# Kernel tuning notes

Hardware: AMD Instinct MI355X
Metric: run time of the kernel (lower is better)

## Reference

```python
import jax, jax.numpy as jnp
import numpy as np


def setup_inputs() -> dict:
    key = jax.random.key(0)
    ks = jax.random.split(key, 4)
    B, C, H, W = 4, 512, 64, 64
    A = 512  # attention_dim
    x = jax.random.normal(ks[0], (B, C, H, W), dtype=jnp.float32)
    # 1x1 conv weights as [out_ch, in_ch] matrices (kaiming-like scale)
    scale = np.sqrt(2.0 / C).astype(np.float32)
    Wq = jax.random.normal(ks[1], (A, C), dtype=jnp.float32) * scale
    Wk = jax.random.normal(ks[2], (A, C), dtype=jnp.float32) * scale
    Wv = jax.random.normal(ks[3], (C, C), dtype=jnp.float32) * scale
    bq = jnp.zeros((A,), dtype=jnp.float32)
    bk = jnp.zeros((A,), dtype=jnp.float32)
    bv = jnp.zeros((C,), dtype=jnp.float32)
    return {"x": x, "Wq": Wq, "bq": bq, "Wk": Wk, "bk": bk, "Wv": Wv, "bv": bv}


def reference(x, Wq, bq, Wk, bk, Wv, bv):
    B, C, H, W = x.shape
    N = H * W
    xf = x.reshape(B, C, N)  # [B, C, N]
    # 1x1 convs == per-pixel channel matmuls
    q = jnp.einsum('ac,bcn->bna', Wq, xf) + bq[None, None, :]   # [B, N, A] (query, permuted)
    k = jnp.einsum('ac,bcn->ban', Wk, xf) + bk[None, :, None]   # [B, A, N] (key)
    v = jnp.einsum('oc,bcn->bno', Wv, xf) + bv[None, None, :]   # [B, N, C] (value, permuted)
    attn = jnp.einsum('bna,bam->bnm', q, k)                     # [B, N, N]
    attn = jax.nn.softmax(attn, axis=-2)                        # softmax over dim=-2 (queries)
    out = jnp.einsum('bnm,bmc->bnc', attn, v)                   # [B, N, C]
    # Faithful to torch: .view(B, C, H, W) reinterprets the [B, N, C] buffer
    out = out.reshape(B, C, H, W)
    return x + 0.1 * out
```

## Files before the change

kernel.cpp:

```cpp
#include <hip/hip_runtime.h>
#include <stdint.h>


#define LDT 40
#define SUB 5120

typedef _Float16 f16x8 __attribute__((ext_vector_type(8)));
typedef float f32x4 __attribute__((ext_vector_type(4)));

template <int ASRC, int EPI, int NSUB>
__global__ void __launch_bounds__(256, 2) gemm_f16(
    const _Float16* __restrict__ Ap, long lda, long zsa,
    const _Float16* __restrict__ Bp, long ldb, long zsb,
    int kslice,
    const _Float16* __restrict__ fs16, long zsl,
    float* __restrict__ outF, _Float16* __restrict__ outH, long ldc, long zso,
    const float* __restrict__ bias0, const float* __restrict__ bias1,
    const float* __restrict__ xadd,
    float* __restrict__ pmax, float* __restrict__ psum, long zsp,
    float alpha)
{
  __shared__ _Float16 smem[2 * NSUB * SUB];

  const int z = blockIdx.z;
  const long i0 = (long)blockIdx.x * 128;
  const long j0 = (long)blockIdx.y * 128;
  const int t = (int)threadIdx.x;
  const int lane = t & 63;
  const int wv = t >> 6;
  const int quad = lane >> 4;
  const int lrow = lane & 15;
  const int wm = (wv & 1) << 6;
  const int wn = (wv >> 1) << 6;

  const int r0 = t >> 2;
  const int s0 = (t & 3) << 3;

  const _Float16* gA0 = Ap + z * zsa + (i0 + r0) * lda + s0;
  const _Float16* gA1 = gA0 + 64 * lda;
  const _Float16* gB0 = Bp + z * zsb + (j0 + r0) * ldb + s0;
  const _Float16* gB1 = gB0 + 64 * ldb;
  const int la0 = r0 * LDT + s0;
  const int la1 = (r0 + 64) * LDT + s0;

  const _Float16* fsZ = nullptr;
  if constexpr (ASRC == 1)
    fsZ = fs16 + z * zsl + (long)blockIdx.x * 4096 + s0;

  f32x4 acc[4][4];
  const f32x4 fz = {0.f, 0.f, 0.f, 0.f};
#pragma unroll
  for (int a = 0; a < 4; a++)
#pragma unroll
    for (int b = 0; b < 4; b++) acc[a][b] = fz;

  for (int kk = 0; kk < kslice; kk += 32 * NSUB) {
    f16x8 va[NSUB][2], vb[NSUB][2];
#pragma unroll
    for (int s = 0; s < NSUB; s++) {
      va[s][0] = *(const f16x8*)(gA0 + kk + 32 * s);
      va[s][1] = *(const f16x8*)(gA1 + kk + 32 * s);
      vb[s][0] = *(const f16x8*)(gB0 + kk + 32 * s);
      vb[s][1] = *(const f16x8*)(gB1 + kk + 32 * s);
    }
    if constexpr (ASRC == 1) {
#pragma unroll
      for (int s = 0; s < NSUB; s++) {
        const f16x8 fsv = *(const f16x8*)(fsZ + kk + 32 * s);
        va[s][0] = va[s][0] * fsv;
        va[s][1] = va[s][1] * fsv;
      }
    }
    __syncthreads();
#pragma unroll
    for (int s = 0; s < NSUB; s++) {
      *(f16x8*)&smem[s * SUB + la0] = va[s][0];
      *(f16x8*)&smem[s * SUB + la1] = va[s][1];
      *(f16x8*)&smem[(NSUB + s) * SUB + la0] = vb[s][0];
      *(f16x8*)&smem[(NSUB + s) * SUB + la1] = vb[s][1];
    }
    __syncthreads();

#pragma unroll
    for (int h = 0; h < NSUB; h++) {
      const _Float16* pA = smem + h * SUB;
      const _Float16* pB = smem + (NSUB + h) * SUB;
      f16x8 fa[4], fb[4];
#pragma unroll
      for (int f = 0; f < 4; f++) {
        fa[f] = *(const f16x8*)&pA[(wm + f * 16 + lrow) * LDT + quad * 8];
        fb[f] = *(const f16x8*)&pB[(wn + f * 16 + lrow) * LDT + quad * 8];
      }
#pragma unroll
      for (int fm = 0; fm < 4; fm++)
#pragma unroll
        for (int fn = 0; fn < 4; fn++)
          acc[fm][fn] = __builtin_amdgcn_mfma_f32_16x16x32_f16(fa[fm], fb[fn], acc[fm][fn], 0, 0, 0);
    }
  }

  const long obase = (long)z * zso;

  if constexpr (EPI == 1 || EPI == 2) {
#pragma unroll
    for (int fm = 0; fm < 4; fm++) {
      const long gi0 = i0 + wm + fm * 16 + quad * 4;
#pragma unroll
      for (int fn = 0; fn < 4; fn++) {
        const long gj = j0 + wn + fn * 16 + lrow;
        float badd = 0.f;
        if constexpr (EPI == 1) badd = (gj < 512) ? bias0[gj] : bias1[gj - 512];
#pragma unroll
        for (int r = 0; r < 4; r++) {
          float v = acc[fm][fn][r];
          if constexpr (EPI == 1) v += badd;
          else v += bias0[gi0 + r];
          outH[obase + (gi0 + r) * ldc + gj] = (_Float16)v;
        }
      }
    }
  } else if constexpr (EPI == 3) {
#pragma unroll
    for (int fm = 0; fm < 4; fm++) {
      const long gi0 = i0 + wm + fm * 16 + quad * 4;
#pragma unroll
      for (int fn = 0; fn < 4; fn++) {
        const long gj = j0 + wn + fn * 16 + lrow;
#pragma unroll
        for (int r = 0; r < 4; r++) {
          const long o = obase + (gi0 + r) * ldc + gj;
          outF[o] = fmaf(alpha, acc[fm][fn][r], xadd[o]);
        }
      }
    }
  } else {
    __syncthreads();
    float* Ls = (float*)smem;
#pragma unroll
    for (int fn = 0; fn < 4; fn++) {
      float mx = -3.4e38f;
#pragma unroll
      for (int fm = 0; fm < 4; fm++)
#pragma unroll
        for (int r = 0; r < 4; r++) mx = fmaxf(mx, acc[fm][fn][r]);
      Ls[(wv * 4 + quad) * 64 + fn * 16 + lrow] = mx;
    }
    __syncthreads();
    {
      const int c = t & 127;
      const int h = t >> 7;
      const int wvv = ((c >> 6) << 1) + h;
      const int wc = c & 63;
      float M = -3.4e38f;
#pragma unroll
      for (int q = 0; q < 4; q++) M = fmaxf(M, Ls[(wvv * 4 + q) * 64 + wc]);
      Ls[1024 + h * 128 + c] = M;
    }
    __syncthreads();
    if (t < 128) {
      float Mcol = fmaxf(Ls[1024 + t], Ls[1152 + t]);
      pmax[z * zsp + (long)blockIdx.x * 4096 + j0 + t] = Mcol;
      Ls[1280 + t] = Mcol;
    }
    __syncthreads();
#pragma unroll
    for (int fn = 0; fn < 4; fn++) {
      const int colc = wn + fn * 16 + lrow;
      const float Mcol = Ls[1280 + colc];
      const long gj = j0 + colc;
      float sm = 0.f;
#pragma unroll
      for (int fm = 0; fm < 4; fm++) {
        const long gi0 = i0 + wm + fm * 16 + quad * 4;
#pragma unroll
        for (int r = 0; r < 4; r++) {
          float e = __expf(acc[fm][fn][r] - Mcol);
          sm += e;
          outH[obase + (gi0 + r) * ldc + gj] = (_Float16)e;
        }
      }
      Ls[(wv * 4 + quad) * 64 + fn * 16 + lrow] = sm;
    }
    __syncthreads();
    if (t < 128) {
      const int wc = t & 63;
      const int ch = t >> 6;
      float s = 0.f;
#pragma unroll
      for (int h = 0; h < 2; h++) {
        const int wvv = (ch << 1) + h;
#pragma unroll
        for (int q = 0; q < 4; q++) s += Ls[(wvv * 4 + q) * 64 + wc];
      }
      psum[z * zsp + (long)blockIdx.x * 4096 + j0 + t] = s;
    }
  }
}

__global__ void convert_weights(const float* __restrict__ Wq, const float* __restrict__ Wk,
                                const float* __restrict__ Wv,
                                _Float16* __restrict__ WQK, _Float16* __restrict__ Wv16)
{
  int idx = blockIdx.x * 256 + threadIdx.x;
  if (idx < 524288)
    WQK[idx] = (_Float16)((idx < 262144) ? Wq[idx] : Wk[idx - 262144]);
  else
    Wv16[idx - 524288] = (_Float16)Wv[idx - 524288];
}

__global__ void transpose_x(const float* __restrict__ x, _Float16* __restrict__ xT)
{
  __shared__ float tile[32][33];
  const int b = blockIdx.z;
  const int n0 = blockIdx.x * 32;
  const int c0 = blockIdx.y * 32;
  const int tx = threadIdx.x;
  const int ty = threadIdx.y;
  const float* xb = x + (long)b * 2097152;
#pragma unroll
  for (int k = 0; k < 4; k++)
    tile[ty + k * 8][tx] = xb[(long)(c0 + ty + k * 8) * 4096 + n0 + tx];
  __syncthreads();
  _Float16* xTb = xT + (long)b * 2097152;
#pragma unroll
  for (int k = 0; k < 4; k++)
    xTb[(long)(n0 + ty + k * 8) * 512 + c0 + tx] = (_Float16)tile[tx][ty + k * 8];
}

__global__ void stats_scale(const float* __restrict__ pmax, const float* __restrict__ psum,
                            _Float16* __restrict__ fs16)
{
  const int idx = blockIdx.x * 256 + threadIdx.x;
  const int z = idx >> 12;
  const int m = idx & 4095;
  const float* pm = pmax + (long)z * 131072 + m;
  const float* ps = psum + (long)z * 131072 + m;
  float M = -3.4e38f, S = 0.f;
  for (int i = 0; i < 32; i++) {
    float m2 = pm[(long)i * 4096], s2 = ps[(long)i * 4096];
    float nm = fmaxf(M, m2);
    S = S * __expf(M - nm) + s2 * __expf(m2 - nm);
    M = nm;
  }
  const float lse = M + __logf(S);
  _Float16* fo = fs16 + (long)z * 131072 + m;
  for (int i = 0; i < 32; i++)
    fo[(long)i * 4096] = (_Float16)__expf(pm[(long)i * 4096] - lse);
}

extern "C" void kernel_launch(void* const* d_in, const int* in_sizes, int n_in,
                              void* d_out, int out_size, void* d_ws, size_t ws_size,
                              hipStream_t stream)
{
  const float* x  = (const float*)d_in[0];
  const float* Wq = (const float*)d_in[1];
  const float* bq = (const float*)d_in[2];
  const float* Wk = (const float*)d_in[3];
  const float* bk = (const float*)d_in[4];
  const float* Wv = (const float*)d_in[5];
  const float* bv = (const float*)d_in[6];
  float* out = (float*)d_out;

  char* w = (char*)d_ws;
  _Float16* WQK   = (_Float16*)(w + 0);
  _Float16* Wv16  = (_Float16*)(w + 1048576);
  _Float16* xT    = (_Float16*)(w + 1572864);
  _Float16* QK    = (_Float16*)(w + 18350080);
  _Float16* Vt    = (_Float16*)(w + 51904512);
  float*    pmaxB = (float*)   (w + 68747264);
  float*    psumB = (float*)   (w + 70844416);
  _Float16* fs16  = (_Float16*)(w + 72941568);
  _Float16* S16   = (_Float16*)(w + 75038720);

  convert_weights<<<3072, 256, 0, stream>>>(Wq, Wk, Wv, WQK, Wv16);
  transpose_x<<<dim3(128, 16, 4), dim3(32, 8), 0, stream>>>(x, xT);

  gemm_f16<0, 1, 2><<<dim3(32, 8, 4), 256, 0, stream>>>(
      xT, 512, 2097152L, WQK, 512, 0L, 512, nullptr, 0L,
      nullptr, QK, 1024, 4194304L, bq, bk, nullptr, nullptr, nullptr, 0L, 0.f);
  gemm_f16<0, 2, 2><<<dim3(4, 32, 4), 256, 0, stream>>>(
      Wv16, 512, 0L, xT, 512, 2097152L, 512, nullptr, 0L,
      nullptr, Vt, 4096, 2097152L, bv, nullptr, nullptr, nullptr, nullptr, 0L, 0.f);
  gemm_f16<0, 4, 2><<<dim3(32, 32, 4), 256, 0, stream>>>(
      QK, 1024, 4194304L, QK + 512, 1024, 4194304L, 512, nullptr, 0L,
      nullptr, S16, 4096, 16777216L, nullptr, nullptr, nullptr,
      pmaxB, psumB, 131072L, 0.f);
  stats_scale<<<64, 256, 0, stream>>>(pmaxB, psumB, fs16);
  gemm_f16<1, 3, 4><<<dim3(32, 4, 4), 256, 0, stream>>>(
      S16, 4096, 16777216L, Vt, 4096, 2097152L, 4096, fs16, 131072L,
      out, nullptr, 512, 2097152L, nullptr, nullptr, x, nullptr, nullptr, 0L, 0.1f);
}
```

Before: 311.4 us.

## Split final attention-value GEMM along K into two partials plus combine kernel

The final S·V GEMM previously ran 512 blocks over a K of 4096. It now splits K into two halves, launching 1024 blocks that write fp16 partial results into the reused QK buffer. A new combine kernel sums the partials and applies the 0.1 scale and residual add. NSUB also drops from 4 to 2, lowering shared memory per block. This is meant to improve occupancy and parallelism, at the cost of an extra kernel launch, extra partial-buffer traffic, and fp16 rounding of the partials.

```diff
diff --git a/kernel.cpp b/kernel.cpp
--- a/kernel.cpp
+++ b/kernel.cpp
@@ -8,7 +8,7 @@
 typedef _Float16 f16x8 __attribute__((ext_vector_type(8)));
 typedef float f32x4 __attribute__((ext_vector_type(4)));
 
-template <int ASRC, int EPI, int NSUB>
+template <int ASRC, int EPI, int NSUB, int SPLITK>
 __global__ void __launch_bounds__(256, 2) gemm_f16(
     const _Float16* __restrict__ Ap, long lda, long zsa,
     const _Float16* __restrict__ Bp, long ldb, long zsb,
@@ -22,7 +22,9 @@
 {
   __shared__ _Float16 smem[2 * NSUB * SUB];
 
-  const int z = blockIdx.z;
+  const int bz = blockIdx.z;
+  const int z = bz / SPLITK;
+  const long koff = (long)(bz % SPLITK) * kslice;
   const long i0 = (long)blockIdx.x * 128;
   const long j0 = (long)blockIdx.y * 128;
   const int t = (int)threadIdx.x;
@@ -36,16 +38,16 @@
   const int r0 = t >> 2;
   const int s0 = (t & 3) << 3;
 
-  const _Float16* gA0 = Ap + z * zsa + (i0 + r0) * lda + s0;
+  const _Float16* gA0 = Ap + z * zsa + (i0 + r0) * lda + s0 + koff;
   const _Float16* gA1 = gA0 + 64 * lda;
-  const _Float16* gB0 = Bp + z * zsb + (j0 + r0) * ldb + s0;
+  const _Float16* gB0 = Bp + z * zsb + (j0 + r0) * ldb + s0 + koff;
   const _Float16* gB1 = gB0 + 64 * ldb;
   const int la0 = r0 * LDT + s0;
   const int la1 = (r0 + 64) * LDT + s0;
 
   const _Float16* fsZ = nullptr;
   if constexpr (ASRC == 1)
-    fsZ = fs16 + z * zsl + (long)blockIdx.x * 4096 + s0;
+    fsZ = fs16 + z * zsl + (long)blockIdx.x * 4096 + s0 + koff;
 
   f32x4 acc[4][4];
   const f32x4 fz = {0.f, 0.f, 0.f, 0.f};
@@ -131,6 +133,19 @@
           const long o = obase + (gi0 + r) * ldc + gj;
           outF[o] = fmaf(alpha, acc[fm][fn][r], xadd[o]);
         }
+      }
+    }
+  } else if constexpr (EPI == 5) {
+    const long pbase = (long)bz * zso;
+#pragma unroll
+    for (int fm = 0; fm < 4; fm++) {
+      const long gi0 = i0 + wm + fm * 16 + quad * 4;
+#pragma unroll
+      for (int fn = 0; fn < 4; fn++) {
+        const long gj = j0 + wn + fn * 16 + lrow;
+#pragma unroll
+        for (int r = 0; r < 4; r++)
+          outH[pbase + (gi0 + r) * ldc + gj] = (_Float16)acc[fm][fn][r];
       }
     }
   } else {
@@ -248,6 +263,30 @@
     fo[(long)i * 4096] = (_Float16)__expf(pm[(long)i * 4096] - lse);
 }
 
+__global__ void combine_splitk(const _Float16* __restrict__ part, const float* __restrict__ x,
+                               float* __restrict__ out)
+{
+  const long i8 = (long)blockIdx.x * 256 + threadIdx.x;
+  const long z = i8 >> 18;
+  const long oz = (i8 & 262143) << 3;
+  const long o = z * 2097152 + oz;
+  const f16x8 p0 = *(const f16x8*)(part + (z * 2) * 2097152 + oz);
+  const f16x8 p1 = *(const f16x8*)(part + (z * 2 + 1) * 2097152 + oz);
+  const float4 x0 = *(const float4*)(x + o);
+  const float4 x1 = *(const float4*)(x + o + 4);
+  float4 o0, o1;
+  o0.x = fmaf(0.1f, (float)p0[0] + (float)p1[0], x0.x);
+  o0.y = fmaf(0.1f, (float)p0[1] + (float)p1[1], x0.y);
+  o0.z = fmaf(0.1f, (float)p0[2] + (float)p1[2], x0.z);
+  o0.w = fmaf(0.1f, (float)p0[3] + (float)p1[3], x0.w);
+  o1.x = fmaf(0.1f, (float)p0[4] + (float)p1[4], x1.x);
+  o1.y = fmaf(0.1f, (float)p0[5] + (float)p1[5], x1.y);
+  o1.z = fmaf(0.1f, (float)p0[6] + (float)p1[6], x1.z);
+  o1.w = fmaf(0.1f, (float)p0[7] + (float)p1[7], x1.w);
+  *(float4*)(out + o) = o0;
+  *(float4*)(out + o + 4) = o1;
+}
+
 extern "C" void kernel_launch(void* const* d_in, const int* in_sizes, int n_in,
                               void* d_out, int out_size, void* d_ws, size_t ws_size,
                               hipStream_t stream)
@@ -266,6 +305,7 @@
   _Float16* Wv16  = (_Float16*)(w + 1048576);
   _Float16* xT    = (_Float16*)(w + 1572864);
   _Float16* QK    = (_Float16*)(w + 18350080);
+  _Float16* part  = QK;
   _Float16* Vt    = (_Float16*)(w + 51904512);
   float*    pmaxB = (float*)   (w + 68747264);
   float*    psumB = (float*)   (w + 70844416);
@@ -275,18 +315,19 @@
   convert_weights<<<3072, 256, 0, stream>>>(Wq, Wk, Wv, WQK, Wv16);
   transpose_x<<<dim3(128, 16, 4), dim3(32, 8), 0, stream>>>(x, xT);
 
-  gemm_f16<0, 1, 2><<<dim3(32, 8, 4), 256, 0, stream>>>(
+  gemm_f16<0, 1, 2, 1><<<dim3(32, 8, 4), 256, 0, stream>>>(
       xT, 512, 2097152L, WQK, 512, 0L, 512, nullptr, 0L,
       nullptr, QK, 1024, 4194304L, bq, bk, nullptr, nullptr, nullptr, 0L, 0.f);
-  gemm_f16<0, 2, 2><<<dim3(4, 32, 4), 256, 0, stream>>>(
+  gemm_f16<0, 2, 2, 1><<<dim3(4, 32, 4), 256, 0, stream>>>(
       Wv16, 512, 0L, xT, 512, 2097152L, 512, nullptr, 0L,
       nullptr, Vt, 4096, 2097152L, bv, nullptr, nullptr, nullptr, nullptr, 0L, 0.f);
-  gemm_f16<0, 4, 2><<<dim3(32, 32, 4), 256, 0, stream>>>(
+  gemm_f16<0, 4, 2, 1><<<dim3(32, 32, 4), 256, 0, stream>>>(
       QK, 1024, 4194304L, QK + 512, 1024, 4194304L, 512, nullptr, 0L,
       nullptr, S16, 4096, 16777216L, nullptr, nullptr, nullptr,
       pmaxB, psumB, 131072L, 0.f);
   stats_scale<<<64, 256, 0, stream>>>(pmaxB, psumB, fs16);
-  gemm_f16<1, 3, 4><<<dim3(32, 4, 4), 256, 0, stream>>>(
-      S16, 4096, 16777216L, Vt, 4096, 2097152L, 4096, fs16, 131072L,
-      out, nullptr, 512, 2097152L, nullptr, nullptr, x, nullptr, nullptr, 0L, 0.1f);
-}
+  gemm_f16<1, 5, 2, 2><<<dim3(32, 4, 8), 256, 0, stream>>>(
+      S16, 4096, 16777216L, Vt, 4096, 2097152L, 2048, fs16, 131072L,
+      nullptr, part, 512, 2097152L, nullptr, nullptr, nullptr, nullptr, nullptr, 0L, 0.f);
+  combine_splitk<<<4096, 256, 0, stream>>>(part, x, out);
+}
```

New measurement: 321.8 us. +3.3%, slower.
